# Kernel optimization log

Hardware: AMD Instinct MI355X
Metric: run time of the kernel (lower is better)

## Reference

```python
import jax, jax.numpy as jnp
import numpy as np

IN_BW = 4
W_BW = 4
EPS = 1e-5


def quantize(x, bw):
    # k-bit uniform quantizer on [-1, 1 - 2^(1-bw)] with straight-through rounding
    scale = 2.0 ** (bw - 1)
    xc = jnp.clip(x, -1.0, 1.0 - 1.0 / scale)
    q = jnp.round(xc * scale) / scale
    return xc + jax.lax.stop_gradient(q - xc)


def bconv(x, w, stride):
    # BinarizeConv2d: quantize activations (in_bw) and weights (weight_bw), then conv
    return jax.lax.conv_general_dilated(
        quantize(x, IN_BW), quantize(w, W_BW),
        window_strides=stride, padding='VALID',
        dimension_numbers=('NCHW', 'OIHW', 'NCHW'))


def bn2d(x, g, b):
    mean = x.mean(axis=(0, 2, 3), keepdims=True)
    var = x.var(axis=(0, 2, 3), keepdims=True)
    return (x - mean) * jax.lax.rsqrt(var + EPS) * g.reshape(1, -1, 1, 1) + b.reshape(1, -1, 1, 1)


def bn1d(x, g, b):
    mean = x.mean(axis=0, keepdims=True)
    var = x.var(axis=0, keepdims=True)
    return (x - mean) * jax.lax.rsqrt(var + EPS) * g + b


def htanh(x):
    return jnp.clip(x, -1.0, 1.0)


def setup_inputs() -> dict:
    key = jax.random.key(0)
    ks = jax.random.split(key, 24)
    B = 8192
    d = {'x': jax.random.normal(ks[0], (B, 1, 1250, 1), dtype=jnp.float32)}
    # conv weights OIHW
    shapes = [(3, 1, 6, 1), (5, 3, 5, 1), (10, 5, 4, 1), (20, 10, 4, 1), (20, 20, 4, 1)]
    for i, s in enumerate(shapes):
        d[f'w{i+1}'] = 0.3 * jax.random.normal(ks[1 + i], s, dtype=jnp.float32)
    d['fw1'] = 0.3 * jax.random.normal(ks[6], (10, 740), dtype=jnp.float32)
    d['fw2'] = 0.3 * jax.random.normal(ks[7], (2, 10), dtype=jnp.float32)
    chans = [3, 5, 10, 20, 20, 10, 2]
    for i, c in enumerate(chans):
        d[f'g{i+1}'] = 1.0 + 0.1 * jax.random.normal(ks[8 + i], (c,), dtype=jnp.float32)
        d[f'b{i+1}'] = 0.1 * jax.random.normal(ks[15 + i], (c,), dtype=jnp.float32)
    return d


def reference(x, w1, w2, w3, w4, w5, fw1, fw2,
              g1, g2, g3, g4, g5, g6, g7,
              b1, b2, b3, b4, b5, b6, b7):
    h = htanh(bn2d(bconv(x, w1, (2, 1)), g1, b1))
    h = htanh(bn2d(bconv(h, w2, (2, 1)), g2, b2))
    h = htanh(bn2d(bconv(h, w3, (2, 1)), g3, b3))
    h = htanh(bn2d(bconv(h, w4, (2, 1)), g4, b4))
    h = htanh(bn2d(bconv(h, w5, (2, 1)), g5, b5))
    h = h.reshape(h.shape[0], -1)  # (B, 20*37*1) = (B, 740)
    # dropout is identity in eval mode
    h = htanh(bn1d(quantize(h, IN_BW) @ quantize(fw1, W_BW).T, g6, b6))
    h = bn1d(quantize(h, IN_BW) @ quantize(fw2, W_BW).T, g7, b7)
    return h
```

## Files before the change

kernel.cpp:

```cpp
#include <hip/hip_runtime.h>

#define DEV __device__ __forceinline__

DEV float qwt(float w) {
    float y = fminf(fmaxf(w, -1.0f), 0.875f);
    return rintf(y * 8.0f) * 0.125f;
}
DEV int qw8i(float w) {
    float y = fminf(fmaxf(w, -1.0f), 0.875f);
    return (int)rintf(y * 8.0f);
}
DEV int q8i(float x, float a, float b) {
    float y = fmaf(x, a, b);
    y = fminf(fmaxf(y, -1.0f), 0.875f);
    return (int)rintf(y * 8.0f);
}
DEV float qact(float x, float a, float b) {
    float y = fmaf(x, a, b);
    y = fminf(fmaxf(y, -1.0f), 0.875f);
    return rintf(y * 8.0f) * 0.125f;
}

DEV int dot4(int a, int b, int c) {
#if __has_builtin(__builtin_amdgcn_sdot4)
    return __builtin_amdgcn_sdot4(a, b, c, false);
#else
    c += (int)(signed char)(a)       * (int)(signed char)(b);
    c += (int)(signed char)(a >> 8)  * (int)(signed char)(b >> 8);
    c += (int)(signed char)(a >> 16) * (int)(signed char)(b >> 16);
    c += (int)(signed char)(a >> 24) * (int)(signed char)(b >> 24);
    return c;
#endif
}
DEV unsigned alignpair(unsigned hi, unsigned lo, int bits) {
#if __has_builtin(__builtin_amdgcn_alignbit)
    return __builtin_amdgcn_alignbit(hi, lo, bits);
#else
    return bits ? ((lo >> bits) | (hi << (32 - bits))) : lo;
#endif
}

DEV void atomAddF64(double* p, double v) { atomicAdd(p, v); }

DEV void pack_layer(const float* w, int* o, int CIN, int COUT, int K, int t) {
    int KW = (K + 3) / 4;
    for (int i = t; i < COUT * CIN * KW; i += 256) {
        int j = i % KW, cc = i / KW;
        unsigned r = 0;
        for (int u = 0; u < 4; u++) {
            int k = 4 * j + u;
            int b = (k < K) ? (qw8i(w[cc * K + k]) & 0xff) : 0;
            r |= (unsigned)b << (8 * u);
        }
        o[i] = (int)r;
    }
}

template<int CIN,int COUT,int K,int LINP,int LOUT,int LOUTP,int P,int R,bool IN_FLOAT,int LIN=0>
DEV void conv_phase(
    const void* __restrict__ in_, const int* __restrict__ wqi,
    const double* __restrict__ statsIn,
    const float* __restrict__ gprev, const float* __restrict__ bprev, double Nprev,
    short* __restrict__ out, double* __restrict__ statsOut, int B, int VB,
    const float* __restrict__ wown,
    const float* __restrict__ pw2, const float* __restrict__ pw3,
    const float* __restrict__ pw4, const float* __restrict__ pw5,
    int* __restrict__ owp2, int* __restrict__ owp3,
    int* __restrict__ owp4, int* __restrict__ owp5)
{
    constexpr int KW   = (K + 3) / 4;
    constexpr int NE   = P + 2 * KW - 1;
    constexpr int ND   = (2 * (NE - 1) + 3) / 4 + 2;
    constexpr int LO_P = (LOUT + P - 1) / P;
    constexpr int GROUPS = R * LO_P;

    __shared__ __align__(16) signed char smem[R * CIN * LINP + 32];
    __shared__ float ts[CIN], tb[CIN];
    __shared__ float red[4][2 * COUT];
    __shared__ int lwq[IN_FLOAT ? (COUT * CIN * KW) : 1];

    const int tid = threadIdx.x;
    const int bid = blockIdx.x;
    const int lane = tid & 63, wid = tid >> 6;

    if constexpr (IN_FLOAT) {
        for (int i = tid; i < COUT * CIN * KW; i += 256) {
            int j = i % KW, cc = i / KW;
            unsigned rr = 0;
            for (int u = 0; u < 4; u++) {
                int k = 4 * j + u;
                int bv = (k < K) ? (qw8i(wown[cc * K + k]) & 0xff) : 0;
                rr |= (unsigned)bv << (8 * u);
            }
            lwq[i] = (int)rr;
        }
        if (bid == 0) {
            pack_layer(pw2, owp2, 3, 5, 5, tid);
            pack_layer(pw3, owp3, 5, 10, 4, tid);
            pack_layer(pw4, owp4, 10, 20, 4, tid);
            pack_layer(pw5, owp5, 20, 20, 4, tid);
        }
    } else {
        if (tid < CIN) {
            double S = 0.0, Q = 0.0;
#pragma unroll
            for (int s = 0; s < 8; s++) {
                S += statsIn[s * (2 * CIN) + 2 * tid];
                Q += statsIn[s * (2 * CIN) + 2 * tid + 1];
            }
            double mean = S / Nprev;
            double var  = Q / Nprev - mean * mean;
            double inv  = 1.0 / sqrt(var + 1e-5);
            double sc   = (double)gprev[tid] * inv;
            ts[tid] = (float)sc * 0.015625f;
            tb[tid] = (float)((double)bprev[tid] - mean * sc);
        }
    }
    __syncthreads();

#pragma unroll 1
    for (int vb = bid; vb < VB; vb += gridDim.x) {
        const int r0   = vb * R;
        const int rcnt = min(R, B - r0);

        if constexpr (IN_FLOAT) {
            constexpr int CH = LIN / 2;
            const float2* gp = (const float2*)in_;
            for (int c = tid; c < rcnt * CH; c += 256) {
                int r = c / CH, rem = c - r * CH;
                float2 v = gp[(size_t)(r0 + r) * CH + rem];
                int b0 = q8i(v.x, 1.f, 0.f) & 0xff;
                int b1 = q8i(v.y, 1.f, 0.f) & 0xff;
                *(unsigned short*)(smem + r * LINP + rem * 2) =
                    (unsigned short)(b0 | (b1 << 8));
            }
        } else {
            constexpr int CH  = CIN * LINP / 8;
            constexpr int CHC = LINP / 8;
            const int4* gp = (const int4*)((const short*)in_ + (size_t)r0 * CIN * LINP);
            for (int c = tid; c < rcnt * CH; c += 256) {
                int rem = c % CH;
                int ci = rem / CHC;
                float a = ts[ci], bo = tb[ci];
                int4 v = gp[c];
                int vs[4] = { v.x, v.y, v.z, v.w };
                unsigned pk[2];
#pragma unroll
                for (int u = 0; u < 2; u++) {
                    unsigned pp = 0;
#pragma unroll
                    for (int j = 0; j < 2; j++) {
                        int word = vs[u * 2 + j];
                        int b0 = q8i((float)(short)(word & 0xffff), a, bo) & 0xff;
                        int b1 = q8i((float)(short)(word >> 16),    a, bo) & 0xff;
                        pp |= (unsigned)(b0 | (b1 << 8)) << (16 * j);
                    }
                    pk[u] = pp;
                }
                ((uint2*)smem)[c] = make_uint2(pk[0], pk[1]);
            }
        }
        __syncthreads();

        float tsum[COUT], tsq[COUT];
#pragma unroll
        for (int c = 0; c < COUT; c++) { tsum[c] = 0.f; tsq[c] = 0.f; }

#pragma unroll 1
        for (int g = tid; g < GROUPS; g += 256) {
            int r = g / LO_P;
            if (r >= rcnt) continue;
            int l0   = (g - r * LO_P) * P;
            int pact = min(P, LOUT - l0);

            int acc[COUT][P];
#pragma unroll
            for (int co = 0; co < COUT; co++)
#pragma unroll
                for (int p = 0; p < P; p++) acc[co][p] = 0;

            const int ibase = r * CIN * LINP + 2 * l0;
            const int sh    = (P % 2 == 0) ? 0 : (ibase & 3);

            for (int ci = 0; ci < CIN; ci++) {
                const int* sp = (const int*)smem + ((ci * LINP + (ibase & ~3)) >> 2);
                int d[ND];
#pragma unroll
                for (int j = 0; j < ND; j++) d[j] = sp[j];
                int e[NE];
#pragma unroll
                for (int i = 0; i < NE; i++) {
                    int off = sh + 2 * i;
                    e[i] = (int)alignpair((unsigned)d[off / 4 + 1], (unsigned)d[off / 4], (off & 3) * 8);
                }
#pragma unroll
                for (int co = 0; co < COUT; co++) {
#pragma unroll
                    for (int j = 0; j < KW; j++) {
                        int wv;
                        if constexpr (IN_FLOAT) wv = lwq[(co * CIN + ci) * KW + j];
                        else                    wv = wqi[(co * CIN + ci) * KW + j];
#pragma unroll
                        for (int p = 0; p < P; p++)
                            acc[co][p] = dot4(e[p + 2 * j], wv, acc[co][p]);
                    }
                }
            }

            const size_t ob = (size_t)(r0 + r) * COUT * LOUTP + l0;
#pragma unroll
            for (int co = 0; co < COUT; co++) {
                if (pact == P) {
                    short tmp[P];
#pragma unroll
                    for (int p = 0; p < P; p++) {
                        tmp[p] = (short)acc[co][p];
                        float v = (float)acc[co][p] * 0.015625f;
                        tsum[co] += v;
                        tsq[co]   = fmaf(v, v, tsq[co]);
                    }
                    short* op = &out[ob + (size_t)co * LOUTP];
                    if constexpr (P == 1) {
                        op[0] = tmp[0];
                    } else if constexpr (P == 2) {
                        *(short2*)op = make_short2(tmp[0], tmp[1]);
                    } else if constexpr (P == 4) {
                        *(short4*)op = make_short4(tmp[0], tmp[1], tmp[2], tmp[3]);
                    } else if constexpr (P == 8) {
                        *(short4*)op       = make_short4(tmp[0], tmp[1], tmp[2], tmp[3]);
                        *(short4*)(op + 4) = make_short4(tmp[4], tmp[5], tmp[6], tmp[7]);
                    }
                } else {
#pragma unroll
                    for (int p = 0; p < P; p++) {
                        if (p < pact) {
                            int k = acc[co][p];
                            out[ob + (size_t)co * LOUTP + p] = (short)k;
                            float v = (float)k * 0.015625f;
                            tsum[co] += v;
                            tsq[co]   = fmaf(v, v, tsq[co]);
                        }
                    }
                }
            }
        }

#pragma unroll
        for (int co = 0; co < COUT; co++) {
            float s = tsum[co], q = tsq[co];
            for (int off = 32; off > 0; off >>= 1) {
                s += __shfl_down(s, off, 64);
                q += __shfl_down(q, off, 64);
            }
            if (lane == 0) { red[wid][2 * co] = s; red[wid][2 * co + 1] = q; }
        }
        __syncthreads();
        if (tid < 2 * COUT) {
            float v = red[0][tid] + red[1][tid] + red[2][tid] + red[3][tid];
            atomAddF64(&statsOut[(size_t)(vb & 7) * (2 * COUT) + tid], (double)v);
        }
        __syncthreads();
    }
}

__global__ __launch_bounds__(256) void k_conv1(
    const float* x, short* y1, double* sl1, int B, int VB,
    const float* w1, const float* w2, const float* w3, const float* w4,
    const float* w5, int* wp2, int* wp3, int* wp4, int* wp5)
{
    conv_phase<1, 3, 6, 1252, 623, 624, 8, 3, true, 1250>(
        x, nullptr, nullptr, nullptr, nullptr, 0.0, y1, sl1, B, VB,
        w1, w2, w3, w4, w5, wp2, wp3, wp4, wp5);
}
__global__ __launch_bounds__(256) void k_conv2(
    const short* in_, const int* wq, const double* sIn,
    const float* g, const float* b, short* out, double* sOut, int B, int VB)
{
    conv_phase<3, 5, 5, 624, 310, 312, 4, 4, false>(
        in_, wq, sIn, g, b, 8192.0 * 623.0, out, sOut, B, VB,
        nullptr, nullptr, nullptr, nullptr, nullptr, nullptr, nullptr, nullptr, nullptr);
}
__global__ __launch_bounds__(256) void k_conv3(
    const short* in_, const int* wq, const double* sIn,
    const float* g, const float* b, short* out, double* sOut, int B, int VB)
{
    conv_phase<5, 10, 4, 312, 154, 160, 2, 4, false>(
        in_, wq, sIn, g, b, 8192.0 * 310.0, out, sOut, B, VB,
        nullptr, nullptr, nullptr, nullptr, nullptr, nullptr, nullptr, nullptr, nullptr);
}
__global__ __launch_bounds__(256) void k_conv4(
    const short* in_, const int* wq, const double* sIn,
    const float* g, const float* b, short* out, double* sOut, int B, int VB)
{
    conv_phase<10, 20, 4, 160, 76, 80, 1, 4, false>(
        in_, wq, sIn, g, b, 8192.0 * 154.0, out, sOut, B, VB,
        nullptr, nullptr, nullptr, nullptr, nullptr, nullptr, nullptr, nullptr, nullptr);
}
__global__ __launch_bounds__(256) void k_conv5(
    const short* in_, const int* wq, const double* sIn,
    const float* g, const float* b, short* out, double* sOut, int B, int VB)
{
    conv_phase<20, 20, 4, 80, 37, 40, 1, 8, false>(
        in_, wq, sIn, g, b, 8192.0 * 76.0, out, sOut, B, VB,
        nullptr, nullptr, nullptr, nullptr, nullptr, nullptr, nullptr, nullptr, nullptr);
}

__global__ __launch_bounds__(256) void k_fc1(
    const short* __restrict__ y5, const float* __restrict__ fw1,
    const double* __restrict__ statsIn,
    const float* __restrict__ g5, const float* __restrict__ b5,
    float* __restrict__ z1, double* __restrict__ statsOut, int B)
{
    __shared__ float wq[7400];
    __shared__ float ts[20], tb[20];
    __shared__ float red[4][20];

    const int tid = threadIdx.x;
    const int bid = blockIdx.x;
    const int lane = tid & 63, wid = tid >> 6;

    for (int i = tid; i < 7400; i += 256) wq[i] = qwt(fw1[i]);
    if (tid < 20) {
        double S = 0.0, Q = 0.0;
#pragma unroll
        for (int s = 0; s < 8; s++) {
            S += statsIn[s * 40 + 2 * tid];
            Q += statsIn[s * 40 + 2 * tid + 1];
        }
        double N = 8192.0 * 37.0;
        double mean = S / N;
        double var  = Q / N - mean * mean;
        double inv  = 1.0 / sqrt(var + 1e-5);
        double sc   = (double)g5[tid] * inv;
        ts[tid] = (float)sc;
        tb[tid] = (float)((double)b5[tid] - mean * sc);
    }
    __syncthreads();

#pragma unroll 1
    for (int r = bid * 4 + wid; r < B; r += gridDim.x * 4) {
        const short* xr = y5 + (size_t)r * 800;
        float acc[10];
#pragma unroll
        for (int j = 0; j < 10; j++) acc[j] = 0.f;
#pragma unroll 1
        for (int f = lane; f < 740; f += 64) {
            int c = f / 37, pos = f - c * 37;
            float x = qact((float)xr[c * 40 + pos] * 0.015625f, ts[c], tb[c]);
#pragma unroll
            for (int j = 0; j < 10; j++) acc[j] = fmaf(x, wq[j * 740 + f], acc[j]);
        }
#pragma unroll
        for (int j = 0; j < 10; j++) {
            float v = acc[j];
            for (int off = 1; off < 64; off <<= 1) v += __shfl_xor(v, off, 64);
            if (lane == j) z1[(size_t)r * 10 + j] = v;
            if (lane == 0) { red[wid][2 * j] = v; red[wid][2 * j + 1] = v * v; }
        }
        __syncthreads();
        if (tid < 20) {
            float v = red[0][tid] + red[1][tid] + red[2][tid] + red[3][tid];
            atomAddF64(&statsOut[(size_t)(bid & 7) * 20 + tid], (double)v);
        }
        __syncthreads();
    }
}

__global__ __launch_bounds__(256) void k_fc2(
    const float* __restrict__ z1, const float* __restrict__ fw2,
    const double* __restrict__ statsIn,
    const float* __restrict__ g6, const float* __restrict__ b6,
    const float* __restrict__ g7, const float* __restrict__ b7,
    float* __restrict__ outp, int B)
{
    __shared__ float zbuf[16384];
    __shared__ float ts7[10], tb7[10], wq2[20];
    __shared__ float fr[4][4];
    __shared__ float tr8[4];

    const int tid = threadIdx.x;
    const int lane = tid & 63, wid = tid >> 6;

    if (tid < 20) wq2[tid] = qwt(fw2[tid]);
    if (tid < 10) {
        double S = 0.0, Q = 0.0;
#pragma unroll
        for (int s = 0; s < 8; s++) {
            S += statsIn[s * 20 + 2 * tid];
            Q += statsIn[s * 20 + 2 * tid + 1];
        }
        double N = 8192.0;
        double mean = S / N;
        double var  = Q / N - mean * mean;
        double inv  = 1.0 / sqrt(var + 1e-5);
        double sc   = (double)g6[tid] * inv;
        ts7[tid] = (float)sc;
        tb7[tid] = (float)((double)b6[tid] - mean * sc);
    }
    __syncthreads();

    float s0 = 0.f, q0 = 0.f, s1 = 0.f, q1 = 0.f;
#pragma unroll 1
    for (int r = tid; r < B; r += 256) {
        float a0 = 0.f, a1 = 0.f;
#pragma unroll
        for (int i = 0; i < 10; i++) {
            float x = qact(z1[(size_t)r * 10 + i], ts7[i], tb7[i]);
            a0 = fmaf(x, wq2[i], a0);
            a1 = fmaf(x, wq2[10 + i], a1);
        }
        zbuf[r * 2]     = a0;
        zbuf[r * 2 + 1] = a1;
        s0 += a0; q0 = fmaf(a0, a0, q0);
        s1 += a1; q1 = fmaf(a1, a1, q1);
    }
    for (int off = 32; off > 0; off >>= 1) {
        s0 += __shfl_down(s0, off, 64); q0 += __shfl_down(q0, off, 64);
        s1 += __shfl_down(s1, off, 64); q1 += __shfl_down(q1, off, 64);
    }
    if (lane == 0) { fr[wid][0] = s0; fr[wid][1] = q0; fr[wid][2] = s1; fr[wid][3] = q1; }
    __syncthreads();
    if (tid < 2) {
        double S = 0.0, Q = 0.0;
        for (int w = 0; w < 4; w++) { S += (double)fr[w][2 * tid]; Q += (double)fr[w][2 * tid + 1]; }
        double N = (double)B;
        double mean = S / N;
        double var  = Q / N - mean * mean;
        double inv  = 1.0 / sqrt(var + 1e-5);
        double sc   = (double)g7[tid] * inv;
        tr8[tid]     = (float)sc;
        tr8[2 + tid] = (float)((double)b7[tid] - mean * sc);
    }
    __syncthreads();
    for (int i = tid; i < 2 * B; i += 256) {
        int c = i & 1;
        outp[i] = fmaf(zbuf[i], tr8[c], tr8[2 + c]);
    }
}

extern "C" void kernel_launch(void* const* d_in, const int* in_sizes, int n_in,
                              void* d_out, int out_size, void* d_ws, size_t ws_size,
                              hipStream_t stream)
{
    const float* x   = (const float*)d_in[0];
    const float* w1  = (const float*)d_in[1];
    const float* w2  = (const float*)d_in[2];
    const float* w3  = (const float*)d_in[3];
    const float* w4  = (const float*)d_in[4];
    const float* w5  = (const float*)d_in[5];
    const float* fw1 = (const float*)d_in[6];
    const float* fw2 = (const float*)d_in[7];
    const float *g[7], *bb[7];
    for (int i = 0; i < 7; i++) { g[i] = (const float*)d_in[8 + 2 * i]; bb[i] = (const float*)d_in[9 + 2 * i]; }

    char* ws = (char*)d_ws;
    size_t off = 0;
    auto alloc = [&](size_t bytes) -> void* {
        void* q = ws + off;
        off += (bytes + 255) & ~(size_t)255;
        return q;
    };
    short* y1 = (short*)alloc((size_t)8192 * 3 * 624 * 2);
    short* y2 = (short*)alloc((size_t)8192 * 5 * 312 * 2);
    short* y3 = (short*)alloc((size_t)8192 * 10 * 160 * 2);
    short* y4 = (short*)alloc((size_t)8192 * 20 * 80 * 2);
    short* y5 = (short*)alloc((size_t)8192 * 20 * 40 * 2);
    float* z1 = (float*)alloc((size_t)81920 * 4);
    int*   wp2 = (int*)alloc(256);  int* wp3 = (int*)alloc(256);
    int*   wp4 = (int*)alloc(1024); int* wp5 = (int*)alloc(2048);
    double* slots = (double*)alloc((size_t)1088 * 8);
    double* sl1 = slots;
    double* sl2 = sl1 + 8 * 6;
    double* sl3 = sl2 + 8 * 10;
    double* sl4 = sl3 + 8 * 20;
    double* sl5 = sl4 + 8 * 40;
    double* sl6 = sl5 + 8 * 40;

    const int B = 8192;

    hipMemsetAsync(slots, 0, (size_t)1088 * 8, stream);

    k_conv1<<<512, 256, 0, stream>>>(x, y1, sl1, B, 2731,
                                     w1, w2, w3, w4, w5, wp2, wp3, wp4, wp5);
    k_conv2<<<512, 256, 0, stream>>>(y1, wp2, sl1, g[0], bb[0], y2, sl2, B, 2048);
    k_conv3<<<512, 256, 0, stream>>>(y2, wp3, sl2, g[1], bb[1], y3, sl3, B, 2048);
    k_conv4<<<512, 256, 0, stream>>>(y3, wp4, sl3, g[2], bb[2], y4, sl4, B, 2048);
    k_conv5<<<512, 256, 0, stream>>>(y4, wp5, sl4, g[3], bb[3], y5, sl5, B, 1024);
    k_fc1<<<1024, 256, 0, stream>>>(y5, fw1, sl5, g[4], bb[4], z1, sl6, B);
    k_fc2<<<1, 256, 0, stream>>>(z1, fw2, sl6, g[5], bb[5], g[6], bb[6],
                                 (float*)d_out, B);
}
```

Measured before the change: 338.2 us.

## Fuse conv2 through fc2 into one cooperative persistent kernel with grid barriers

Replaces the chain of separate launches for conv2–conv5, fc1 and fc2 with one cooperative kernel of 1024 blocks. The stages are separated by a software grid barrier built on sharded atomic counters, and batch-norm statistics are read back with agent-scope atomic loads. The aim is to cut kernel launch gaps and the tail idle time between stages. In exchange, stage-1 also moves to 1024 blocks, every block spins at each barrier, and the final fc2 stage runs on a single block while the rest of the grid has exited. If the cooperative launch fails, the code falls back to the old separate launches.

Measured after the change: 919.8 us. 2.72x slower.

```diff
diff --git a/kernel.cpp b/kernel.cpp
--- a/kernel.cpp
+++ b/kernel.cpp
@@ -41,6 +41,9 @@
 }
 
 DEV void atomAddF64(double* p, double v) { atomicAdd(p, v); }
+DEV double aldD(const double* p) {
+    return __hip_atomic_load(p, __ATOMIC_RELAXED, __HIP_MEMORY_SCOPE_AGENT);
+}
 
 DEV void pack_layer(const float* w, int* o, int CIN, int COUT, int K, int t) {
     int KW = (K + 3) / 4;
@@ -438,6 +441,356 @@
     }
 }
 
+struct Params {
+    const float *fw1, *fw2;
+    const float *g1, *b1, *g2, *b2, *g3, *b3, *g4, *b4, *g5, *b5, *g6, *b6, *g7, *b7;
+    const short *y1;
+    short *y2, *y3, *y4, *y5;
+    float *z1, *z2;
+    const int *wp2, *wp3, *wp4, *wp5;
+    double *sl1, *sl2, *sl3, *sl4, *sl5, *sl6;
+    unsigned *bc;
+    float *outp;
+};
+
+DEV void gridbar(unsigned* bc, unsigned target) {
+    __syncthreads();
+    if (threadIdx.x == 0) {
+        atomicAdd(&bc[(blockIdx.x & 7) * 32], 1u);
+        for (;;) {
+            unsigned s = 0;
+#pragma unroll
+            for (int i = 0; i < 8; i++)
+                s += __hip_atomic_load(&bc[i * 32], __ATOMIC_RELAXED,
+                                       __HIP_MEMORY_SCOPE_AGENT);
+            if (s >= target) break;
+            __builtin_amdgcn_s_sleep(8);
+        }
+    }
+    __syncthreads();
+}
+
+template<int CIN>
+DEV void bridgeA(char* SB, const double* sIn, const float* g, const float* b,
+                 double Nprev) {
+    float* ts = (float*)(SB + 13056);
+    float* tb = (float*)(SB + 13184);
+    if (threadIdx.x < CIN) {
+        double S = 0.0, Q = 0.0;
+#pragma unroll
+        for (int s = 0; s < 8; s++) {
+            S += aldD(&sIn[s * (2 * CIN) + 2 * threadIdx.x]);
+            Q += aldD(&sIn[s * (2 * CIN) + 2 * threadIdx.x + 1]);
+        }
+        double mean = S / Nprev;
+        double var  = Q / Nprev - mean * mean;
+        double inv  = 1.0 / sqrt(var + 1e-5);
+        double sc   = (double)g[threadIdx.x] * inv;
+        ts[threadIdx.x] = (float)sc * 0.015625f;
+        tb[threadIdx.x] = (float)((double)b[threadIdx.x] - mean * sc);
+    }
+    __syncthreads();
+}
+
+template<int CIN,int COUT,int K,int LINP,int LOUT,int LOUTP,int P,int R>
+DEV void conv_chunk(char* SB, const short* in_, const int* wqi,
+                    short* out, double* statsOut, int vb, int B)
+{
+    constexpr int KW   = (K + 3) / 4;
+    constexpr int NE   = P + 2 * KW - 1;
+    constexpr int ND   = (2 * (NE - 1) + 3) / 4 + 2;
+    constexpr int LO_P = (LOUT + P - 1) / P;
+    constexpr int GROUPS = R * LO_P;
+
+    signed char* smem = (signed char*)SB;
+    float* ts  = (float*)(SB + 13056);
+    float* tb  = (float*)(SB + 13184);
+    float* red = (float*)(SB + 13312);
+
+    const int tid = threadIdx.x;
+    const int lane = tid & 63, wid = tid >> 6;
+    const int r0   = vb * R;
+    const int rcnt = min(R, B - r0);
+
+    {
+        constexpr int CH  = CIN * LINP / 8;
+        constexpr int CHC = LINP / 8;
+        const int4* gp = (const int4*)(in_ + (size_t)r0 * CIN * LINP);
+        for (int c = tid; c < rcnt * CH; c += 256) {
+            int rem = c % CH;
+            int ci = rem / CHC;
+            float a = ts[ci], bo = tb[ci];
+            int4 v = gp[c];
+            int vs[4] = { v.x, v.y, v.z, v.w };
+            unsigned pk[2];
+#pragma unroll
+            for (int u = 0; u < 2; u++) {
+                unsigned pp = 0;
+#pragma unroll
+                for (int j = 0; j < 2; j++) {
+                    int word = vs[u * 2 + j];
+                    int b0 = q8i((float)(short)(word & 0xffff), a, bo) & 0xff;
+                    int b1 = q8i((float)(short)(word >> 16),    a, bo) & 0xff;
+                    pp |= (unsigned)(b0 | (b1 << 8)) << (16 * j);
+                }
+                pk[u] = pp;
+            }
+            ((uint2*)smem)[c] = make_uint2(pk[0], pk[1]);
+        }
+    }
+    __syncthreads();
+
+    float tsum[COUT], tsq[COUT];
+#pragma unroll
+    for (int c = 0; c < COUT; c++) { tsum[c] = 0.f; tsq[c] = 0.f; }
+
+#pragma unroll 1
+    for (int g = tid; g < GROUPS; g += 256) {
+        int r = g / LO_P;
+        if (r >= rcnt) continue;
+        int l0   = (g - r * LO_P) * P;
+        int pact = min(P, LOUT - l0);
+
+        int acc[COUT][P];
+#pragma unroll
+        for (int co = 0; co < COUT; co++)
+#pragma unroll
+            for (int p = 0; p < P; p++) acc[co][p] = 0;
+
+        const int ibase = r * CIN * LINP + 2 * l0;
+        const int sh    = (P % 2 == 0) ? 0 : (ibase & 3);
+
+        for (int ci = 0; ci < CIN; ci++) {
+            const int* sp = (const int*)smem + ((ci * LINP + (ibase & ~3)) >> 2);
+            int d[ND];
+#pragma unroll
+            for (int j = 0; j < ND; j++) d[j] = sp[j];
+            int e[NE];
+#pragma unroll
+            for (int i = 0; i < NE; i++) {
+                int off = sh + 2 * i;
+                e[i] = (int)alignpair((unsigned)d[off / 4 + 1], (unsigned)d[off / 4], (off & 3) * 8);
+            }
+#pragma unroll
+            for (int co = 0; co < COUT; co++) {
+#pragma unroll
+                for (int j = 0; j < KW; j++) {
+                    int wv = wqi[(co * CIN + ci) * KW + j];
+#pragma unroll
+                    for (int p = 0; p < P; p++)
+                        acc[co][p] = dot4(e[p + 2 * j], wv, acc[co][p]);
+                }
+            }
+        }
+
+        const size_t ob = (size_t)(r0 + r) * COUT * LOUTP + l0;
+#pragma unroll
+        for (int co = 0; co < COUT; co++) {
+            if (pact == P) {
+                short tmp[P];
+#pragma unroll
+                for (int p = 0; p < P; p++) {
+                    tmp[p] = (short)acc[co][p];
+                    float v = (float)acc[co][p] * 0.015625f;
+                    tsum[co] += v;
+                    tsq[co]   = fmaf(v, v, tsq[co]);
+                }
+                short* op = &out[ob + (size_t)co * LOUTP];
+                if constexpr (P == 1) {
+                    op[0] = tmp[0];
+                } else if constexpr (P == 2) {
+                    *(short2*)op = make_short2(tmp[0], tmp[1]);
+                } else if constexpr (P == 4) {
+                    *(short4*)op = make_short4(tmp[0], tmp[1], tmp[2], tmp[3]);
+                } else if constexpr (P == 8) {
+                    *(short4*)op       = make_short4(tmp[0], tmp[1], tmp[2], tmp[3]);
+                    *(short4*)(op + 4) = make_short4(tmp[4], tmp[5], tmp[6], tmp[7]);
+                }
+            } else {
+#pragma unroll
+                for (int p = 0; p < P; p++) {
+                    if (p < pact) {
+                        int k = acc[co][p];
+                        out[ob + (size_t)co * LOUTP + p] = (short)k;
+                        float v = (float)k * 0.015625f;
+                        tsum[co] += v;
+                        tsq[co]   = fmaf(v, v, tsq[co]);
+                    }
+                }
+            }
+        }
+    }
+
+#pragma unroll
+    for (int co = 0; co < COUT; co++) {
+        float s = tsum[co], q = tsq[co];
+        for (int off = 32; off > 0; off >>= 1) {
+            s += __shfl_down(s, off, 64);
+            q += __shfl_down(q, off, 64);
+        }
+        if (lane == 0) { red[wid * 2 * COUT + 2 * co] = s; red[wid * 2 * COUT + 2 * co + 1] = q; }
+    }
+    __syncthreads();
+    if (tid < 2 * COUT) {
+        float v = red[tid] + red[2 * COUT + tid] + red[4 * COUT + tid] + red[6 * COUT + tid];
+        atomAddF64(&statsOut[(size_t)(vb & 7) * (2 * COUT) + tid], (double)v);
+    }
+    __syncthreads();
+}
+
+__global__ __launch_bounds__(256, 4) void k_fused(Params p)
+{
+    __shared__ double SBd[3840];
+    char* SB = (char*)SBd;
+    const int b   = blockIdx.x;
+    const int tid = threadIdx.x;
+    const int lane = tid & 63, wid = tid >> 6;
+    const int B = 8192;
+
+    bridgeA<3>(SB, p.sl1, p.g1, p.b1, 8192.0 * 623.0);
+    conv_chunk<3, 5, 5, 624, 310, 312, 4, 4>(SB, p.y1, p.wp2, p.y2, p.sl2, 2 * b,     B);
+    conv_chunk<3, 5, 5, 624, 310, 312, 4, 4>(SB, p.y1, p.wp2, p.y2, p.sl2, 2 * b + 1, B);
+    gridbar(p.bc, 1 * 1024);
+
+    bridgeA<5>(SB, p.sl2, p.g2, p.b2, 8192.0 * 310.0);
+    conv_chunk<5, 10, 4, 312, 154, 160, 2, 4>(SB, p.y2, p.wp3, p.y3, p.sl3, 2 * b,     B);
+    conv_chunk<5, 10, 4, 312, 154, 160, 2, 4>(SB, p.y2, p.wp3, p.y3, p.sl3, 2 * b + 1, B);
+    gridbar(p.bc, 2 * 1024);
+
+    bridgeA<10>(SB, p.sl3, p.g3, p.b3, 8192.0 * 154.0);
+    conv_chunk<10, 20, 4, 160, 76, 80, 1, 4>(SB, p.y3, p.wp4, p.y4, p.sl4, 2 * b,     B);
+    conv_chunk<10, 20, 4, 160, 76, 80, 1, 4>(SB, p.y3, p.wp4, p.y4, p.sl4, 2 * b + 1, B);
+    gridbar(p.bc, 3 * 1024);
+
+    bridgeA<20>(SB, p.sl4, p.g4, p.b4, 8192.0 * 76.0);
+    conv_chunk<20, 20, 4, 80, 37, 40, 1, 8>(SB, p.y4, p.wp5, p.y5, p.sl5, b, B);
+    gridbar(p.bc, 4 * 1024);
+
+    {
+        float* wq  = (float*)SB;
+        float* ts  = (float*)(SB + 29600);
+        float* tb  = (float*)(SB + 29696);
+        float* red = (float*)(SB + 29792);
+
+        for (int i = tid; i < 7400; i += 256) wq[i] = qwt(p.fw1[i]);
+        if (tid < 20) {
+            double S = 0.0, Q = 0.0;
+#pragma unroll
+            for (int s = 0; s < 8; s++) {
+                S += aldD(&p.sl5[s * 40 + 2 * tid]);
+                Q += aldD(&p.sl5[s * 40 + 2 * tid + 1]);
+            }
+            double N = 8192.0 * 37.0;
+            double mean = S / N;
+            double var  = Q / N - mean * mean;
+            double inv  = 1.0 / sqrt(var + 1e-5);
+            double sc   = (double)p.g5[tid] * inv;
+            ts[tid] = (float)sc;
+            tb[tid] = (float)((double)p.b5[tid] - mean * sc);
+        }
+        __syncthreads();
+
+#pragma unroll 1
+        for (int it = 0; it < 2; it++) {
+            int r = 8 * b + 4 * it + wid;
+            const short* xr = p.y5 + (size_t)r * 800;
+            float acc[10];
+#pragma unroll
+            for (int j = 0; j < 10; j++) acc[j] = 0.f;
+#pragma unroll 1
+            for (int f = lane; f < 740; f += 64) {
+                int c = f / 37, pos = f - c * 37;
+                float x = qact((float)xr[c * 40 + pos] * 0.015625f, ts[c], tb[c]);
+#pragma unroll
+                for (int j = 0; j < 10; j++) acc[j] = fmaf(x, wq[j * 740 + f], acc[j]);
+            }
+#pragma unroll
+            for (int j = 0; j < 10; j++) {
+                float v = acc[j];
+                for (int off = 1; off < 64; off <<= 1) v += __shfl_xor(v, off, 64);
+                if (lane == j)
+                    __hip_atomic_store(&p.z1[(size_t)r * 10 + j], v,
+                                       __ATOMIC_RELAXED, __HIP_MEMORY_SCOPE_AGENT);
+                if (lane == 0) { red[wid * 20 + 2 * j] = v; red[wid * 20 + 2 * j + 1] = v * v; }
+            }
+            __syncthreads();
+            if (tid < 20) {
+                float v = red[tid] + red[20 + tid] + red[40 + tid] + red[60 + tid];
+                atomAddF64(&p.sl6[(size_t)((2 * b + it) & 7) * 20 + tid], (double)v);
+            }
+            __syncthreads();
+        }
+    }
+    gridbar(p.bc, 5 * 1024);
+
+    if (b != 0) return;
+    {
+        float* ts7 = (float*)SB;
+        float* tb7 = (float*)(SB + 64);
+        float* wq2 = (float*)(SB + 128);
+        float* fr  = (float*)(SB + 256);
+        float* tr8 = (float*)(SB + 512);
+
+        if (tid < 20) wq2[tid] = qwt(p.fw2[tid]);
+        if (tid < 10) {
+            double S = 0.0, Q = 0.0;
+#pragma unroll
+            for (int s = 0; s < 8; s++) {
+                S += aldD(&p.sl6[s * 20 + 2 * tid]);
+                Q += aldD(&p.sl6[s * 20 + 2 * tid + 1]);
+            }
+            double N = 8192.0;
+            double mean = S / N;
+            double var  = Q / N - mean * mean;
+            double inv  = 1.0 / sqrt(var + 1e-5);
+            double sc   = (double)p.g6[tid] * inv;
+            ts7[tid] = (float)sc;
+            tb7[tid] = (float)((double)p.b6[tid] - mean * sc);
+        }
+        __syncthreads();
+
+        float s0 = 0.f, q0 = 0.f, s1 = 0.f, q1 = 0.f;
+#pragma unroll 1
+        for (int r = tid; r < B; r += 256) {
+            float a0 = 0.f, a1 = 0.f;
+#pragma unroll
+            for (int i = 0; i < 10; i++) {
+                float zv = __hip_atomic_load(&p.z1[(size_t)r * 10 + i],
+                                             __ATOMIC_RELAXED, __HIP_MEMORY_SCOPE_AGENT);
+                float x = qact(zv, ts7[i], tb7[i]);
+                a0 = fmaf(x, wq2[i], a0);
+                a1 = fmaf(x, wq2[10 + i], a1);
+            }
+            p.z2[r * 2]     = a0;
+            p.z2[r * 2 + 1] = a1;
+            s0 += a0; q0 = fmaf(a0, a0, q0);
+            s1 += a1; q1 = fmaf(a1, a1, q1);
+        }
+        for (int off = 32; off > 0; off >>= 1) {
+            s0 += __shfl_down(s0, off, 64); q0 += __shfl_down(q0, off, 64);
+            s1 += __shfl_down(s1, off, 64); q1 += __shfl_down(q1, off, 64);
+        }
+        if (lane == 0) { fr[wid * 4 + 0] = s0; fr[wid * 4 + 1] = q0; fr[wid * 4 + 2] = s1; fr[wid * 4 + 3] = q1; }
+        __syncthreads();
+        if (tid < 2) {
+            double S = 0.0, Q = 0.0;
+            for (int w = 0; w < 4; w++) { S += (double)fr[w * 4 + 2 * tid]; Q += (double)fr[w * 4 + 2 * tid + 1]; }
+            double N = (double)B;
+            double mean = S / N;
+            double var  = Q / N - mean * mean;
+            double inv  = 1.0 / sqrt(var + 1e-5);
+            double sc   = (double)p.g7[tid] * inv;
+            tr8[tid]     = (float)sc;
+            tr8[2 + tid] = (float)((double)p.b7[tid] - mean * sc);
+        }
+        __syncthreads();
+        for (int i = tid; i < 2 * B; i += 256) {
+            int c = i & 1;
+            p.outp[i] = fmaf(p.z2[i], tr8[c], tr8[2 + c]);
+        }
+    }
+}
+
 extern "C" void kernel_launch(void* const* d_in, const int* in_sizes, int n_in,
                               void* d_out, int out_size, void* d_ws, size_t ws_size,
                               hipStream_t stream)
@@ -466,27 +819,50 @@
     short* y4 = (short*)alloc((size_t)8192 * 20 * 80 * 2);
     short* y5 = (short*)alloc((size_t)8192 * 20 * 40 * 2);
     float* z1 = (float*)alloc((size_t)81920 * 4);
+    float* z2 = (float*)alloc((size_t)8192 * 2 * 4);
     int*   wp2 = (int*)alloc(256);  int* wp3 = (int*)alloc(256);
     int*   wp4 = (int*)alloc(1024); int* wp5 = (int*)alloc(2048);
-    double* slots = (double*)alloc((size_t)1088 * 8);
+    double* slots = (double*)alloc((size_t)1088 * 8 + 1024);
     double* sl1 = slots;
     double* sl2 = sl1 + 8 * 6;
     double* sl3 = sl2 + 8 * 10;
     double* sl4 = sl3 + 8 * 20;
     double* sl5 = sl4 + 8 * 40;
     double* sl6 = sl5 + 8 * 40;
+    unsigned* bc = (unsigned*)(sl6 + 8 * 20);
 
     const int B = 8192;
 
-    hipMemsetAsync(slots, 0, (size_t)1088 * 8, stream);
-
-    k_conv1<<<512, 256, 0, stream>>>(x, y1, sl1, B, 2731,
-                                     w1, w2, w3, w4, w5, wp2, wp3, wp4, wp5);
-    k_conv2<<<512, 256, 0, stream>>>(y1, wp2, sl1, g[0], bb[0], y2, sl2, B, 2048);
-    k_conv3<<<512, 256, 0, stream>>>(y2, wp3, sl2, g[1], bb[1], y3, sl3, B, 2048);
-    k_conv4<<<512, 256, 0, stream>>>(y3, wp4, sl3, g[2], bb[2], y4, sl4, B, 2048);
-    k_conv5<<<512, 256, 0, stream>>>(y4, wp5, sl4, g[3], bb[3], y5, sl5, B, 1024);
-    k_fc1<<<1024, 256, 0, stream>>>(y5, fw1, sl5, g[4], bb[4], z1, sl6, B);
-    k_fc2<<<1, 256, 0, stream>>>(z1, fw2, sl6, g[5], bb[5], g[6], bb[6],
-                                 (float*)d_out, B);
-}
+    hipMemsetAsync(slots, 0, (size_t)1088 * 8 + 1024, stream);
+
+    k_conv1<<<1024, 256, 0, stream>>>(x, y1, sl1, B, 2731,
+                                      w1, w2, w3, w4, w5, wp2, wp3, wp4, wp5);
+
+    Params hp;
+    hp.fw1 = fw1; hp.fw2 = fw2;
+    hp.g1 = g[0]; hp.b1 = bb[0]; hp.g2 = g[1]; hp.b2 = bb[1];
+    hp.g3 = g[2]; hp.b3 = bb[2]; hp.g4 = g[3]; hp.b4 = bb[3];
+    hp.g5 = g[4]; hp.b5 = bb[4]; hp.g6 = g[5]; hp.b6 = bb[5];
+    hp.g7 = g[6]; hp.b7 = bb[6];
+    hp.y1 = y1; hp.y2 = y2; hp.y3 = y3; hp.y4 = y4; hp.y5 = y5;
+    hp.z1 = z1; hp.z2 = z2;
+    hp.wp2 = wp2; hp.wp3 = wp3; hp.wp4 = wp4; hp.wp5 = wp5;
+    hp.sl1 = sl1; hp.sl2 = sl2; hp.sl3 = sl3; hp.sl4 = sl4;
+    hp.sl5 = sl5; hp.sl6 = sl6;
+    hp.bc = bc;
+    hp.outp = (float*)d_out;
+
+    void* args[] = { &hp };
+    hipError_t e = hipLaunchCooperativeKernel((const void*)k_fused, dim3(1024),
+                                              dim3(256), args, 0u, stream);
+    if (e != hipSuccess) {
+        (void)hipGetLastError();
+        k_conv2<<<1024, 256, 0, stream>>>(y1, wp2, sl1, g[0], bb[0], y2, sl2, B, 2048);
+        k_conv3<<<1024, 256, 0, stream>>>(y2, wp3, sl2, g[1], bb[1], y3, sl3, B, 2048);
+        k_conv4<<<1024, 256, 0, stream>>>(y3, wp4, sl3, g[2], bb[2], y4, sl4, B, 2048);
+        k_conv5<<<1024, 256, 0, stream>>>(y4, wp5, sl4, g[3], bb[3], y5, sl5, B, 1024);
+        k_fc1<<<1024, 256, 0, stream>>>(y5, fw1, sl5, g[4], bb[4], z1, sl6, B);
+        k_fc2<<<1, 256, 0, stream>>>(z1, fw2, sl6, g[5], bb[5], g[6], bb[6],
+                                     (float*)d_out, B);
+    }
+}
```
